# Optimization experiments

Hardware: AMD Instinct MI355X
Metric: run time of the kernel (lower is better)

The kernel has to match this reference:

```python
import jax, jax.numpy as jnp
import numpy as np

B, S, HID = 2, 2048, 2048
NH, NKV, HD = 16, 4, 128
G = NH // NKV  # kv group size
EPS = 1e-6


def setup_inputs() -> dict:
    key = jax.random.key(0)
    ks = jax.random.split(key, 7)
    w = 0.02
    return {
        "hidden_states": jax.random.normal(ks[0], (B, S, HID), dtype=jnp.float32),
        "position_ids": jnp.broadcast_to(jnp.arange(S, dtype=jnp.int64), (B, S)),
        "Wq": jax.random.normal(ks[1], (2 * NH * HD, HID), dtype=jnp.float32) * w,
        "Wk": jax.random.normal(ks[2], (NKV * HD, HID), dtype=jnp.float32) * w,
        "Wv": jax.random.normal(ks[3], (NKV * HD, HID), dtype=jnp.float32) * w,
        "Wo": jax.random.normal(ks[4], (HID, NH * HD), dtype=jnp.float32) * w,
        "norm_w": jnp.zeros((HID,), dtype=jnp.float32),
    }


def reference(hidden_states, position_ids, Wq, Wk, Wv, Wo, norm_w):
    # RMSNorm (weight parameterized as 1 + w, per source)
    ms = jnp.mean(hidden_states * hidden_states, axis=-1, keepdims=True)
    x = hidden_states * jax.lax.rsqrt(ms + EPS) * (1.0 + norm_w)

    qg = x @ Wq.T                                   # (B,S,2*NH*HD)
    q, gate = jnp.split(qg, 2, axis=-1)
    q = q.reshape(B, S, NH, HD).transpose(0, 2, 1, 3)       # (B,NH,S,HD)
    gate = gate.reshape(B, S, NH, HD).transpose(0, 2, 1, 3)
    k = (x @ Wk.T).reshape(B, S, NKV, HD).transpose(0, 2, 1, 3)  # (B,NKV,S,HD)
    v = (x @ Wv.T).reshape(B, S, NKV, HD).transpose(0, 2, 1, 3)

    scale = 1.0 / np.sqrt(HD).astype(np.float32)
    qg4 = q.reshape(B, NKV, G, S, HD)
    attn = jnp.einsum("bkgqd,bkld->bkgql", qg4, k) * scale   # (B,NKV,G,S,S)
    p = jax.nn.softmax(attn, axis=-1)
    o = jnp.einsum("bkgql,bkld->bkgqd", p, v).reshape(B, NH, S, HD)

    o = o * jax.nn.sigmoid(gate)                    # output gate
    o = o.transpose(0, 2, 1, 3).reshape(B, S, NH * HD)
    return o @ Wo.T
```

## Files before the change

### kernel.cpp

```cpp
#include <hip/hip_runtime.h>
#include <math.h>

#define BB    2
#define SS    2048
#define HIDD  2048
#define NHH   16
#define NKVV  4
#define HDD   128
#define MROWS 4096
#define QG_N  4096
#define KV_N  512
#define O_N   2048
#define KDIM  2048
#define EPS_  1e-6f
#define SCALE_ 0.08838834764831845f

typedef __attribute__((ext_vector_type(8))) __bf16 bf16x8;
typedef __attribute__((ext_vector_type(8))) unsigned short u16x8;
typedef __attribute__((ext_vector_type(4))) float f32x4;

__device__ __forceinline__ unsigned short f2bf(float f) {
  return __builtin_bit_cast(unsigned short, (__bf16)f);
}

__global__ __launch_bounds__(256) void f2bf_k(const float* __restrict__ in,
                                              unsigned short* __restrict__ out, int n4) {
  int i = blockIdx.x * 256 + threadIdx.x;
  if (i < n4) {
    float4 v = ((const float4*)in)[i];
    ushort4 u;
    u.x = f2bf(v.x); u.y = f2bf(v.y); u.z = f2bf(v.z); u.w = f2bf(v.w);
    ((ushort4*)out)[i] = u;
  }
}

__global__ __launch_bounds__(256) void rmsnorm_k(const float* __restrict__ h,
                                                 const float* __restrict__ w,
                                                 unsigned short* __restrict__ x) {
  int row = blockIdx.x;
  int t = threadIdx.x;
  const float4* hr = (const float4*)(h + (size_t)row * HIDD);
  const float4* w4 = (const float4*)w;

  float4 v0 = hr[t], v1 = hr[t + 256];
  float ss = v0.x*v0.x + v0.y*v0.y + v0.z*v0.z + v0.w*v0.w
           + v1.x*v1.x + v1.y*v1.y + v1.z*v1.z + v1.w*v1.w;
#pragma unroll
  for (int off = 32; off > 0; off >>= 1) ss += __shfl_down(ss, off, 64);

  __shared__ float part[4];
  __shared__ float rs_sh;
  if ((t & 63) == 0) part[t >> 6] = ss;
  __syncthreads();
  if (t == 0) rs_sh = rsqrtf((part[0]+part[1]+part[2]+part[3]) * (1.0f/HIDD) + EPS_);
  __syncthreads();
  float rs = rs_sh;

  float4 w0 = w4[t], w1 = w4[t + 256];
  ushort4 o0, o1;
  o0.x = f2bf(v0.x * rs * (1.f + w0.x));
  o0.y = f2bf(v0.y * rs * (1.f + w0.y));
  o0.z = f2bf(v0.z * rs * (1.f + w0.z));
  o0.w = f2bf(v0.w * rs * (1.f + w0.w));
  o1.x = f2bf(v1.x * rs * (1.f + w1.x));
  o1.y = f2bf(v1.y * rs * (1.f + w1.y));
  o1.z = f2bf(v1.z * rs * (1.f + w1.z));
  o1.w = f2bf(v1.w * rs * (1.f + w1.w));
  ushort4* xr = (ushort4*)(x + (size_t)row * HIDD);
  xr[t] = o0;
  xr[t + 256] = o1;
}

template <int OBF>
__device__ __forceinline__ void gemm_core(const unsigned short* __restrict__ Ab,
                                          const unsigned short* __restrict__ Bb,
                                          void* __restrict__ Cv,
                                          void* __restrict__ Cv2,
                                          int Ndim, int bm, int bn,
                                          unsigned short* Als, unsigned short* Bls) {
  char* ldsA = (char*)Als;
  char* ldsB = (char*)Bls;

  int t   = threadIdx.x;
  int r15 = t & 15;
  int g   = (t & 63) >> 4;
  int w   = t >> 6;
  int wr  = w >> 1, wc = w & 1;

  f32x4 acc[4][4] = {};

  for (int k0 = 0; k0 < KDIM; k0 += 64) {
    __syncthreads();
#pragma unroll
    for (int it = 0; it < 4; ++it) {
      int f      = it * 256 + t;
      int row    = f >> 3;
      int schunk = (f & 7) ^ (row & 7);
      unsigned ldsbase = (unsigned)((it * 256 + (w << 6)) << 4);
      __builtin_amdgcn_global_load_lds(
          (const unsigned int*)(Ab + ((size_t)(bm + row) << 11) + k0 + schunk * 8),
          (unsigned int*)(ldsA + ldsbase), 16, 0, 0);
      __builtin_amdgcn_global_load_lds(
          (const unsigned int*)(Bb + ((size_t)(bn + row) << 11) + k0 + schunk * 8),
          (unsigned int*)(ldsB + ldsbase), 16, 0, 0);
    }
    __syncthreads();

#pragma unroll
    for (int tt = 0; tt < 2; ++tt) {
      bf16x8 af[4], bfv[4];
#pragma unroll
      for (int mi = 0; mi < 4; ++mi) {
        int row = wr * 64 + mi * 16 + r15;
        af[mi] = *(const bf16x8*)(ldsA + row * 128 + (((4 * tt + g) ^ (row & 7)) << 4));
      }
#pragma unroll
      for (int ni = 0; ni < 4; ++ni) {
        int row = wc * 64 + ni * 16 + r15;
        bfv[ni] = *(const bf16x8*)(ldsB + row * 128 + (((4 * tt + g) ^ (row & 7)) << 4));
      }
      __builtin_amdgcn_s_setprio(1);
#pragma unroll
      for (int mi = 0; mi < 4; ++mi)
#pragma unroll
        for (int ni = 0; ni < 4; ++ni)
          acc[mi][ni] = __builtin_amdgcn_mfma_f32_16x16x32_bf16(af[mi], bfv[ni], acc[mi][ni], 0, 0, 0);
      __builtin_amdgcn_s_setprio(0);
    }
  }

#pragma unroll
  for (int mi = 0; mi < 4; ++mi)
#pragma unroll
    for (int ni = 0; ni < 4; ++ni) {
      int col = bn + wc * 64 + ni * 16 + r15;
#pragma unroll
      for (int r = 0; r < 4; ++r) {
        int rowg = bm + wr * 64 + mi * 16 + g * 4 + r;
        if (OBF == 1)
          ((unsigned short*)Cv)[(size_t)rowg * Ndim + col] = f2bf(acc[mi][ni][r]);
        else if (OBF == 2) {
          if (col < O_N)
            ((unsigned short*)Cv)[(size_t)rowg * O_N + col] = f2bf(acc[mi][ni][r] * SCALE_);
          else
            ((float*)Cv2)[(size_t)rowg * O_N + (col - O_N)] = acc[mi][ni][r];
        } else
          ((float*)Cv)[(size_t)rowg * Ndim + col] = acc[mi][ni][r];
      }
    }
}

template <int OBF>
__global__ __launch_bounds__(256) void gemm_bf16(const unsigned short* __restrict__ Ab,
                                                 const unsigned short* __restrict__ Bb,
                                                 void* __restrict__ Cv,
                                                 int Ndim) {
  __shared__ unsigned short Als[128 * 64];
  __shared__ unsigned short Bls[128 * 64];
  gemm_core<OBF>(Ab, Bb, Cv, nullptr, Ndim, blockIdx.y * 128, blockIdx.x * 128, Als, Bls);
}

__global__ __launch_bounds__(256) void gemm_qg(const unsigned short* __restrict__ Ab,
                                               const unsigned short* __restrict__ Bb,
                                               unsigned short* __restrict__ Cq,
                                               float* __restrict__ Cg) {
  __shared__ unsigned short Als[128 * 64];
  __shared__ unsigned short Bls[128 * 64];
  gemm_core<2>(Ab, Bb, (void*)Cq, (void*)Cg, QG_N, blockIdx.y * 128, blockIdx.x * 128, Als, Bls);
}

__global__ __launch_bounds__(256) void gemm_kv(const unsigned short* __restrict__ Ab,
                                               const unsigned short* __restrict__ Wk,
                                               const unsigned short* __restrict__ Wv,
                                               unsigned short* __restrict__ Ck,
                                               unsigned short* __restrict__ Cva) {
  __shared__ unsigned short Als[128 * 64];
  __shared__ unsigned short Bls[128 * 64];
  int bx = blockIdx.x;
  const unsigned short* Bb = (bx < 4) ? Wk : Wv;
  unsigned short* Cv = (bx < 4) ? Ck : Cva;
  gemm_core<1>(Ab, Bb, (void*)Cv, nullptr, KV_N, blockIdx.y * 128, (bx & 3) * 128, Als, Bls);
}

__global__ __launch_bounds__(256, 2) void attn_mfma(const unsigned short* __restrict__ qb,
                                                    const float* __restrict__ gateb,
                                                    const unsigned short* __restrict__ kb,
                                                    const unsigned short* __restrict__ vb,
                                                    unsigned short* __restrict__ obuf) {
  __shared__ unsigned short Ks[2][64 * 128];
  __shared__ unsigned short Vt[2][64 * 128];
  char* ldsK0 = (char*)Ks;
  char* ldsV0 = (char*)Vt;

  int t = threadIdx.x;
  int l = t & 63, w = t >> 6;
  int c15 = l & 15, g = l >> 4;
  int bid = blockIdx.x;
  int swz = (bid & 7) * 64 + (bid >> 3);
  int qt = swz & 15, h = (swz >> 4) & 15, b = swz >> 8;
  int kh = h >> 2;
  size_t rowQ0 = (size_t)b * SS + (size_t)qt * 128;
  size_t rowKbase = (size_t)b * SS;

  bf16x8 qf[2][4];
#pragma unroll
  for (int qi = 0; qi < 2; ++qi)
#pragma unroll
    for (int ks = 0; ks < 4; ++ks)
      qf[qi][ks] = *(const bf16x8*)(qb + (rowQ0 + w * 32 + qi * 16 + c15) * O_N
                                       + h * HDD + g * 8 + ks * 32);

  f32x4 accO[2][8] = {};
  float mrun[2] = {-INFINITY, -INFINITY};
  float lrun[2] = {0.f, 0.f};
  u16x8 vreg[4];

#define ISSUE_K(bufi, kt_)                                                     \
  {                                                                            \
    size_t rowK0 = rowKbase + (size_t)(kt_) * 64;                              \
    _Pragma("unroll")                                                          \
    for (int it = 0; it < 4; ++it) {                                           \
      int f = it * 256 + t;                                                    \
      int kv = f >> 4;                                                         \
      int schunk = (f & 15) ^ (kv & 7);                                        \
      unsigned ldsbase = (unsigned)((it * 256 + (w << 6)) << 4);               \
      __builtin_amdgcn_global_load_lds(                                        \
          (const unsigned int*)(kb + (rowK0 + kv) * KV_N + kh * HDD + schunk * 8), \
          (unsigned int*)(ldsK0 + (bufi) * 16384 + ldsbase), 16, 0, 0);        \
    }                                                                          \
  }
#define ISSUE_V(kt_)                                                           \
  {                                                                            \
    size_t rowK0 = rowKbase + (size_t)(kt_) * 64;                              \
    _Pragma("unroll")                                                          \
    for (int it = 0; it < 4; ++it) {                                           \
      int f = it * 256 + t;                                                    \
      int kv = f & 63;                                                         \
      int d8 = (f >> 6) * 8;                                                   \
      vreg[it] = *(const u16x8*)(vb + (rowK0 + kv) * KV_N + kh * HDD + d8);    \
    }                                                                          \
  }
#define WRITE_V(bufi)                                                          \
  {                                                                            \
    _Pragma("unroll")                                                          \
    for (int it = 0; it < 4; ++it) {                                           \
      int f = it * 256 + t;                                                    \
      int kv = f & 63;                                                         \
      int sig = (kv & 32) + ((kv & 12) << 1) + ((kv & 16) >> 2) + (kv & 3);    \
      int d8 = (f >> 6) * 8;                                                   \
      _Pragma("unroll")                                                        \
      for (int i = 0; i < 8; ++i) {                                            \
        int d = d8 + i;                                                        \
        *(unsigned short*)(ldsV0 + (bufi) * 16384 + d * 128 +                  \
                           (((sig >> 3) ^ (d & 7)) << 4) + (sig & 7) * 2) = vreg[it][i]; \
      }                                                                        \
    }                                                                          \
  }

  ISSUE_K(0, 0);
  ISSUE_V(0);
  asm volatile("s_waitcnt vmcnt(0)" ::: "memory");
  WRITE_V(0);
  __syncthreads();

  const int NT = SS / 64;
  for (int kt = 0; kt < NT; ++kt) {
    int cur = kt & 1, nxt = cur ^ 1;
    char* ldsK = ldsK0 + cur * 16384;
    char* ldsV = ldsV0 + cur * 16384;

    if (kt + 1 < NT) {
      ISSUE_K(nxt, kt + 1);
      ISSUE_V(kt + 1);
    }

    f32x4 accS[2][4] = {};
    __builtin_amdgcn_s_setprio(1);
#pragma unroll
    for (int nf = 0; nf < 4; ++nf) {
      int kvr = nf * 16 + c15;
#pragma unroll
      for (int ks = 0; ks < 4; ++ks) {
        bf16x8 kf = *(const bf16x8*)(ldsK + kvr * 256 + ((((g + 4 * ks) ^ (kvr & 7)) << 4)));
#pragma unroll
        for (int qi = 0; qi < 2; ++qi)
          accS[qi][nf] = __builtin_amdgcn_mfma_f32_16x16x32_bf16(kf, qf[qi][ks], accS[qi][nf], 0, 0, 0);
      }
    }
    __builtin_amdgcn_s_setprio(0);

    float mt[2];
#pragma unroll
    for (int qi = 0; qi < 2; ++qi) {
      float m0 = fmaxf(fmaxf(accS[qi][0][0], accS[qi][0][1]), fmaxf(accS[qi][0][2], accS[qi][0][3]));
#pragma unroll
      for (int nf = 1; nf < 4; ++nf)
        m0 = fmaxf(m0, fmaxf(fmaxf(accS[qi][nf][0], accS[qi][nf][1]), fmaxf(accS[qi][nf][2], accS[qi][nf][3])));
      m0 = fmaxf(m0, __shfl_xor(m0, 16, 64));
      m0 = fmaxf(m0, __shfl_xor(m0, 32, 64));
      mt[qi] = m0;
    }

    bool safe = (mt[0] <= mrun[0] + 8.f) && (mt[1] <= mrun[1] + 8.f);
    if (!__all(safe)) {
#pragma unroll
      for (int qi = 0; qi < 2; ++qi) {
        float mnew = fmaxf(mrun[qi], mt[qi]);
        float al = __expf(mrun[qi] - mnew);
        mrun[qi] = mnew;
        lrun[qi] *= al;
        float alr[4];
#pragma unroll
        for (int r = 0; r < 4; ++r) alr[r] = __shfl(al, g * 4 + r, 16);
#pragma unroll
        for (int df = 0; df < 8; ++df)
#pragma unroll
          for (int r = 0; r < 4; ++r) accO[qi][df][r] *= alr[r];
      }
    }

    u16x8 pfr[2][2];
#pragma unroll
    for (int qi = 0; qi < 2; ++qi) {
      float ps = 0.f;
#pragma unroll
      for (int nf = 0; nf < 4; ++nf) {
        float p0 = __expf(accS[qi][nf][0] - mrun[qi]);
        float p1 = __expf(accS[qi][nf][1] - mrun[qi]);
        float p2 = __expf(accS[qi][nf][2] - mrun[qi]);
        float p3 = __expf(accS[qi][nf][3] - mrun[qi]);
        ps += (p0 + p1) + (p2 + p3);
        pfr[qi][nf >> 1][(nf & 1) * 4 + 0] = f2bf(p0);
        pfr[qi][nf >> 1][(nf & 1) * 4 + 1] = f2bf(p1);
        pfr[qi][nf >> 1][(nf & 1) * 4 + 2] = f2bf(p2);
        pfr[qi][nf >> 1][(nf & 1) * 4 + 3] = f2bf(p3);
      }
      ps += __shfl_xor(ps, 16, 64);
      ps += __shfl_xor(ps, 32, 64);
      lrun[qi] += ps;
    }

    __builtin_amdgcn_s_setprio(1);
#pragma unroll
    for (int ks2 = 0; ks2 < 2; ++ks2) {
      bf16x8 pf0 = __builtin_bit_cast(bf16x8, pfr[0][ks2]);
      bf16x8 pf1 = __builtin_bit_cast(bf16x8, pfr[1][ks2]);
#pragma unroll
      for (int df = 0; df < 8; ++df) {
        int d = df * 16 + c15;
        bf16x8 vf = *(const bf16x8*)(ldsV + d * 128 + ((((g + 4 * ks2) ^ (d & 7)) << 4)));
        accO[0][df] = __builtin_amdgcn_mfma_f32_16x16x32_bf16(pf0, vf, accO[0][df], 0, 0, 0);
        accO[1][df] = __builtin_amdgcn_mfma_f32_16x16x32_bf16(pf1, vf, accO[1][df], 0, 0, 0);
      }
    }
    __builtin_amdgcn_s_setprio(0);

    if (kt + 1 < NT) {
      asm volatile("s_waitcnt vmcnt(0)" ::: "memory");
      WRITE_V(nxt);
    }
    __syncthreads();
  }

#pragma unroll
  for (int qi = 0; qi < 2; ++qi) {
    float invL = 1.f / lrun[qi];
    float ivr[4];
#pragma unroll
    for (int r = 0; r < 4; ++r) ivr[r] = __shfl(invL, g * 4 + r, 16);
#pragma unroll
    for (int r = 0; r < 4; ++r) {
      size_t row = rowQ0 + w * 32 + qi * 16 + g * 4 + r;
#pragma unroll
      for (int df = 0; df < 8; ++df) {
        int d = df * 16 + c15;
        float gt = gateb[row * (size_t)O_N + h * HDD + d];
        float sg = 1.f / (1.f + __expf(-gt));
        obuf[row * (size_t)O_N + h * HDD + d] = f2bf(accO[qi][df][r] * ivr[r] * sg);
      }
    }
  }
#undef ISSUE_K
#undef ISSUE_V
#undef WRITE_V
}

extern "C" void kernel_launch(void* const* d_in, const int* in_sizes, int n_in,
                              void* d_out, int out_size, void* d_ws, size_t ws_size,
                              hipStream_t stream) {
  const float* hs = (const float*)d_in[0];
  const float* Wq = (const float*)d_in[2];
  const float* Wk = (const float*)d_in[3];
  const float* Wv = (const float*)d_in[4];
  const float* Wo = (const float*)d_in[5];
  const float* nw = (const float*)d_in[6];
  float* out = (float*)d_out;

  float* gateb = (float*)d_ws;
  unsigned short* qb16 = (unsigned short*)(gateb + (size_t)MROWS * O_N);
  unsigned short* kb16 = qb16 + (size_t)MROWS * O_N;
  unsigned short* vb16 = kb16 + (size_t)MROWS * KV_N;
  unsigned short* xb   = vb16 + (size_t)MROWS * KV_N;
  unsigned short* ob   = xb   + (size_t)MROWS * HIDD;
  unsigned short* wqb  = ob   + (size_t)MROWS * O_N;
  unsigned short* wkb  = wqb  + (size_t)QG_N * KDIM;
  unsigned short* wvb  = wkb  + (size_t)KV_N * KDIM;
  unsigned short* wob  = wvb  + (size_t)KV_N * KDIM;

  f2bf_k<<<(QG_N*KDIM/4 + 255)/256, 256, 0, stream>>>(Wq, wqb, QG_N*KDIM/4);
  f2bf_k<<<(KV_N*KDIM/4 + 255)/256, 256, 0, stream>>>(Wk, wkb, KV_N*KDIM/4);
  f2bf_k<<<(KV_N*KDIM/4 + 255)/256, 256, 0, stream>>>(Wv, wvb, KV_N*KDIM/4);
  f2bf_k<<<(O_N*KDIM/4  + 255)/256, 256, 0, stream>>>(Wo, wob, O_N*KDIM/4);
  rmsnorm_k<<<MROWS, 256, 0, stream>>>(hs, nw, xb);

  gemm_qg<<<dim3(QG_N/128, MROWS/128), 256, 0, stream>>>(xb, wqb, qb16, gateb);
  gemm_kv<<<dim3(8, MROWS/128), 256, 0, stream>>>(xb, wkb, wvb, kb16, vb16);
  attn_mfma<<<dim3(512), 256, 0, stream>>>(qb16, gateb, kb16, vb16, ob);
  gemm_bf16<0><<<dim3(O_N/128, MROWS/128), 256, 0, stream>>>(ob, wob, out, O_N);
}
```

Measured before the change: 286.3 us.

## Write V transposed from KV GEMM and async-load it into LDS in attention

The KV projection GEMM now writes V in a transposed (dim-major, token-contiguous) layout. This lets the attention kernel stream V tiles straight into LDS with global_load_lds, the same way it loads K, instead of loading through registers and doing scattered 2-byte LDS writes after a wait. The four weight-conversion launches are also merged into one kernel. The cost is strided 2-byte stores in the GEMM epilogue for the transposed V, plus two 8-byte LDS reads per V fragment instead of one 16-byte read.

```diff
diff --git a/kernel.cpp b/kernel.cpp
--- a/kernel.cpp
+++ b/kernel.cpp
@@ -23,15 +23,25 @@
   return __builtin_bit_cast(unsigned short, (__bf16)f);
 }
 
-__global__ __launch_bounds__(256) void f2bf_k(const float* __restrict__ in,
-                                              unsigned short* __restrict__ out, int n4) {
+__global__ __launch_bounds__(256) void f2bf_all(const float* __restrict__ Wq,
+                                                const float* __restrict__ Wk,
+                                                const float* __restrict__ Wv,
+                                                const float* __restrict__ Wo,
+                                                unsigned short* __restrict__ dst) {
+  const int s0 = QG_N * KDIM / 4;
+  const int s1 = s0 + KV_N * KDIM / 4;
+  const int s2 = s1 + KV_N * KDIM / 4;
+  const int s3 = s2 + O_N * KDIM / 4;
   int i = blockIdx.x * 256 + threadIdx.x;
-  if (i < n4) {
-    float4 v = ((const float4*)in)[i];
-    ushort4 u;
-    u.x = f2bf(v.x); u.y = f2bf(v.y); u.z = f2bf(v.z); u.w = f2bf(v.w);
-    ((ushort4*)out)[i] = u;
-  }
+  if (i >= s3) return;
+  float4 v;
+  if (i < s0)      v = ((const float4*)Wq)[i];
+  else if (i < s1) v = ((const float4*)Wk)[i - s0];
+  else if (i < s2) v = ((const float4*)Wv)[i - s1];
+  else             v = ((const float4*)Wo)[i - s2];
+  ushort4 u;
+  u.x = f2bf(v.x); u.y = f2bf(v.y); u.z = f2bf(v.z); u.w = f2bf(v.w);
+  ((ushort4*)dst)[i] = u;
 }
 
 __global__ __launch_bounds__(256) void rmsnorm_k(const float* __restrict__ h,
@@ -144,7 +154,9 @@
             ((unsigned short*)Cv)[(size_t)rowg * O_N + col] = f2bf(acc[mi][ni][r] * SCALE_);
           else
             ((float*)Cv2)[(size_t)rowg * O_N + (col - O_N)] = acc[mi][ni][r];
-        } else
+        } else if (OBF == 3)
+          ((unsigned short*)Cv)[(size_t)col * MROWS + rowg] = f2bf(acc[mi][ni][r]);
+        else
           ((float*)Cv)[(size_t)rowg * Ndim + col] = acc[mi][ni][r];
       }
     }
@@ -173,22 +185,23 @@
                                                const unsigned short* __restrict__ Wk,
                                                const unsigned short* __restrict__ Wv,
                                                unsigned short* __restrict__ Ck,
-                                               unsigned short* __restrict__ Cva) {
+                                               unsigned short* __restrict__ Cvt) {
   __shared__ unsigned short Als[128 * 64];
   __shared__ unsigned short Bls[128 * 64];
   int bx = blockIdx.x;
-  const unsigned short* Bb = (bx < 4) ? Wk : Wv;
-  unsigned short* Cv = (bx < 4) ? Ck : Cva;
-  gemm_core<1>(Ab, Bb, (void*)Cv, nullptr, KV_N, blockIdx.y * 128, (bx & 3) * 128, Als, Bls);
+  if (bx < 4)
+    gemm_core<1>(Ab, Wk, (void*)Ck, nullptr, KV_N, blockIdx.y * 128, bx * 128, Als, Bls);
+  else
+    gemm_core<3>(Ab, Wv, (void*)Cvt, nullptr, KV_N, blockIdx.y * 128, (bx & 3) * 128, Als, Bls);
 }
 
 __global__ __launch_bounds__(256, 2) void attn_mfma(const unsigned short* __restrict__ qb,
                                                     const float* __restrict__ gateb,
                                                     const unsigned short* __restrict__ kb,
-                                                    const unsigned short* __restrict__ vb,
+                                                    const unsigned short* __restrict__ vt,
                                                     unsigned short* __restrict__ obuf) {
   __shared__ unsigned short Ks[2][64 * 128];
-  __shared__ unsigned short Vt[2][64 * 128];
+  __shared__ unsigned short Vt[2][128 * 64];
   char* ldsK0 = (char*)Ks;
   char* ldsV0 = (char*)Vt;
 
@@ -213,7 +226,6 @@
   f32x4 accO[2][8] = {};
   float mrun[2] = {-INFINITY, -INFINITY};
   float lrun[2] = {0.f, 0.f};
-  u16x8 vreg[4];
 
 #define ISSUE_K(bufi, kt_)                                                     \
   {                                                                            \
@@ -229,38 +241,24 @@
           (unsigned int*)(ldsK0 + (bufi) * 16384 + ldsbase), 16, 0, 0);        \
     }                                                                          \
   }
-#define ISSUE_V(kt_)                                                           \
+#define ISSUE_VT(bufi, kt_)                                                    \
   {                                                                            \
-    size_t rowK0 = rowKbase + (size_t)(kt_) * 64;                              \
+    size_t tokbase = rowKbase + (size_t)(kt_) * 64;                            \
     _Pragma("unroll")                                                          \
     for (int it = 0; it < 4; ++it) {                                           \
       int f = it * 256 + t;                                                    \
-      int kv = f & 63;                                                         \
-      int d8 = (f >> 6) * 8;                                                   \
-      vreg[it] = *(const u16x8*)(vb + (rowK0 + kv) * KV_N + kh * HDD + d8);    \
+      int row = f >> 3;                                                        \
+      int schunk = (f & 7) ^ (row & 7);                                        \
+      unsigned ldsbase = (unsigned)((it * 256 + (w << 6)) << 4);               \
+      __builtin_amdgcn_global_load_lds(                                        \
+          (const unsigned int*)(vt + (size_t)(kh * 128 + row) * MROWS + tokbase + schunk * 8), \
+          (unsigned int*)(ldsV0 + (bufi) * 16384 + ldsbase), 16, 0, 0);        \
     }                                                                          \
   }
-#define WRITE_V(bufi)                                                          \
-  {                                                                            \
-    _Pragma("unroll")                                                          \
-    for (int it = 0; it < 4; ++it) {                                           \
-      int f = it * 256 + t;                                                    \
-      int kv = f & 63;                                                         \
-      int sig = (kv & 32) + ((kv & 12) << 1) + ((kv & 16) >> 2) + (kv & 3);    \
-      int d8 = (f >> 6) * 8;                                                   \
-      _Pragma("unroll")                                                        \
-      for (int i = 0; i < 8; ++i) {                                            \
-        int d = d8 + i;                                                        \
-        *(unsigned short*)(ldsV0 + (bufi) * 16384 + d * 128 +                  \
-                           (((sig >> 3) ^ (d & 7)) << 4) + (sig & 7) * 2) = vreg[it][i]; \
-      }                                                                        \
-    }                                                                          \
-  }
 
   ISSUE_K(0, 0);
-  ISSUE_V(0);
+  ISSUE_VT(0, 0);
   asm volatile("s_waitcnt vmcnt(0)" ::: "memory");
-  WRITE_V(0);
   __syncthreads();
 
   const int NT = SS / 64;
@@ -271,7 +269,7 @@
 
     if (kt + 1 < NT) {
       ISSUE_K(nxt, kt + 1);
-      ISSUE_V(kt + 1);
+      ISSUE_VT(nxt, kt + 1);
     }
 
     f32x4 accS[2][4] = {};
@@ -345,10 +343,16 @@
     for (int ks2 = 0; ks2 < 2; ++ks2) {
       bf16x8 pf0 = __builtin_bit_cast(bf16x8, pfr[0][ks2]);
       bf16x8 pf1 = __builtin_bit_cast(bf16x8, pfr[1][ks2]);
+      int c0 = 4 * ks2 + (g >> 1);
+      int half8 = (g & 1) * 8;
 #pragma unroll
       for (int df = 0; df < 8; ++df) {
         int d = df * 16 + c15;
-        bf16x8 vf = *(const bf16x8*)(ldsV + d * 128 + ((((g + 4 * ks2) ^ (d & 7)) << 4)));
+        const char* vrow = ldsV + d * 128;
+        ushort4 lo = *(const ushort4*)(vrow + (((c0)     ^ (d & 7)) << 4) + half8);
+        ushort4 hi = *(const ushort4*)(vrow + (((c0 + 2) ^ (d & 7)) << 4) + half8);
+        u16x8 v8 = {lo.x, lo.y, lo.z, lo.w, hi.x, hi.y, hi.z, hi.w};
+        bf16x8 vf = __builtin_bit_cast(bf16x8, v8);
         accO[0][df] = __builtin_amdgcn_mfma_f32_16x16x32_bf16(pf0, vf, accO[0][df], 0, 0, 0);
         accO[1][df] = __builtin_amdgcn_mfma_f32_16x16x32_bf16(pf1, vf, accO[1][df], 0, 0, 0);
       }
@@ -357,7 +361,6 @@
 
     if (kt + 1 < NT) {
       asm volatile("s_waitcnt vmcnt(0)" ::: "memory");
-      WRITE_V(nxt);
     }
     __syncthreads();
   }
@@ -381,8 +384,7 @@
     }
   }
 #undef ISSUE_K
-#undef ISSUE_V
-#undef WRITE_V
+#undef ISSUE_VT
 }
 
 extern "C" void kernel_launch(void* const* d_in, const int* in_sizes, int n_in,
@@ -399,22 +401,20 @@
   float* gateb = (float*)d_ws;
   unsigned short* qb16 = (unsigned short*)(gateb + (size_t)MROWS * O_N);
   unsigned short* kb16 = qb16 + (size_t)MROWS * O_N;
-  unsigned short* vb16 = kb16 + (size_t)MROWS * KV_N;
-  unsigned short* xb   = vb16 + (size_t)MROWS * KV_N;
+  unsigned short* vt16 = kb16 + (size_t)MROWS * KV_N;
+  unsigned short* xb   = vt16 + (size_t)KV_N * MROWS;
   unsigned short* ob   = xb   + (size_t)MROWS * HIDD;
   unsigned short* wqb  = ob   + (size_t)MROWS * O_N;
   unsigned short* wkb  = wqb  + (size_t)QG_N * KDIM;
   unsigned short* wvb  = wkb  + (size_t)KV_N * KDIM;
   unsigned short* wob  = wvb  + (size_t)KV_N * KDIM;
 
-  f2bf_k<<<(QG_N*KDIM/4 + 255)/256, 256, 0, stream>>>(Wq, wqb, QG_N*KDIM/4);
-  f2bf_k<<<(KV_N*KDIM/4 + 255)/256, 256, 0, stream>>>(Wk, wkb, KV_N*KDIM/4);
-  f2bf_k<<<(KV_N*KDIM/4 + 255)/256, 256, 0, stream>>>(Wv, wvb, KV_N*KDIM/4);
-  f2bf_k<<<(O_N*KDIM/4  + 255)/256, 256, 0, stream>>>(Wo, wob, O_N*KDIM/4);
+  const int tot4 = (QG_N + KV_N + KV_N + O_N) * KDIM / 4;
+  f2bf_all<<<(tot4 + 255) / 256, 256, 0, stream>>>(Wq, Wk, Wv, Wo, wqb);
   rmsnorm_k<<<MROWS, 256, 0, stream>>>(hs, nw, xb);
 
   gemm_qg<<<dim3(QG_N/128, MROWS/128), 256, 0, stream>>>(xb, wqb, qb16, gateb);
-  gemm_kv<<<dim3(8, MROWS/128), 256, 0, stream>>>(xb, wkb, wvb, kb16, vb16);
-  attn_mfma<<<dim3(512), 256, 0, stream>>>(qb16, gateb, kb16, vb16, ob);
+  gemm_kv<<<dim3(8, MROWS/128), 256, 0, stream>>>(xb, wkb, wvb, kb16, vt16);
+  attn_mfma<<<dim3(512), 256, 0, stream>>>(qb16, gateb, kb16, vt16, ob);
   gemm_bf16<0><<<dim3(O_N/128, MROWS/128), 256, 0, stream>>>(ob, wob, out, O_N);
 }
```

New measurement: 283.9 us. Within noise of the previous version (-0.8%).
